# Optimization experiments

Hardware: AMD Instinct MI355X
Metric: run time of the kernel (lower is better)

## Reference

```python
import jax, jax.numpy as jnp
import numpy as np

ETA = 0.5  # from init_kwargs; eta >= 0 branch
N = 16777216

def setup_inputs() -> dict:
    key = jax.random.key(0)
    k1, k2 = jax.random.split(key)
    outputs = jax.random.normal(k1, (N,), dtype=jnp.float32)
    # PNU targets in {-1, 0, 1}
    targets = jax.random.randint(k2, (N,), 0, 3, dtype=jnp.int32) - 1
    p_ratio = jnp.array([0.4, 0.6], dtype=jnp.float32)
    return {"outputs": outputs, "targets": targets, "p_ratio": p_ratio}

def reference(outputs, targets, p_ratio):
    y = outputs.reshape(-1)
    t = targets.reshape(-1).astype(y.dtype)

    # masks (computed once, fused)
    idx_p = jnp.maximum(t, 0.0)          # positive examples
    idx_n = jnp.maximum(-t, 0.0)         # negative examples
    idx_u = 1.0 - jnp.abs(t)             # unlabeled examples

    sig_neg = jax.nn.sigmoid(-y)         # loss_func(-y)
    sig_pos = jax.nn.sigmoid(y)          # loss_func(-(-y))

    n_p = jnp.maximum(1.0, jnp.sum(idx_p))
    n_n = jnp.maximum(1.0, jnp.sum(idx_n))
    n_u = jnp.maximum(1.0, jnp.sum(idx_u))

    R_P_plus  = jnp.sum(idx_p * sig_neg) / n_p
    R_P_minus = jnp.sum(idx_p * sig_pos) / n_p
    R_N_minus = jnp.sum(idx_n * sig_pos) / n_n
    R_U_minus = jnp.sum(idx_u * sig_pos) / n_u

    R_PN = p_ratio[0] * R_P_plus + p_ratio[1] * R_N_minus
    R_PU = p_ratio[0] * (R_P_plus - R_P_minus) + R_U_minus

    # eta >= 0 branch
    return (1.0 - ETA) * R_PN + ETA * R_PU
```

## Files before the change

### kernel.cpp

```cpp
#include <hip/hip_runtime.h>

#define ETA 0.5f
#define NBLOCKS 2048
#define NTHREADS 256

__device__ __forceinline__ float wave_reduce_sum(float v) {
#pragma unroll
    for (int off = 32; off > 0; off >>= 1)
        v += __shfl_down(v, off, 64);
    return v;
}

__global__ __launch_bounds__(NTHREADS) void pnu_partial_kernel(
    const float* __restrict__ y, const int* __restrict__ t,
    float* __restrict__ partials, int n, int nblocks) {
    const int nvec = n >> 2;
    const float4* __restrict__ y4 = reinterpret_cast<const float4*>(y);
    const int4* __restrict__ t4 = reinterpret_cast<const int4*>(t);

    float sPp = 0.f, sPm = 0.f, sNm = 0.f, sUm = 0.f;
    float cP = 0.f, cN = 0.f, cU = 0.f;

    const int stride = gridDim.x * blockDim.x;
    for (int i = blockIdx.x * blockDim.x + threadIdx.x; i < nvec; i += stride) {
        float4 yv = y4[i];
        int4 tv = t4[i];
        float ys[4] = {yv.x, yv.y, yv.z, yv.w};
        int   ts[4] = {tv.x, tv.y, tv.z, tv.w};
#pragma unroll
        for (int j = 0; j < 4; ++j) {
            float s = __builtin_amdgcn_rcpf(1.0f + __expf(-ys[j]));
            int tt = ts[j];
            float isP = (tt == 1)  ? 1.0f : 0.0f;
            float isN = (tt == -1) ? 1.0f : 0.0f;
            float isU = (tt == 0)  ? 1.0f : 0.0f;
            sPp += isP * (1.0f - s);
            sPm += isP * s;
            sNm += isN * s;
            sUm += isU * s;
            cP += isP; cN += isN; cU += isU;
        }
    }

    if (blockIdx.x == 0 && threadIdx.x == 0) {
        for (int i = (nvec << 2); i < n; ++i) {
            float s = __builtin_amdgcn_rcpf(1.0f + __expf(-y[i]));
            int tt = t[i];
            float isP = (tt == 1)  ? 1.0f : 0.0f;
            float isN = (tt == -1) ? 1.0f : 0.0f;
            float isU = (tt == 0)  ? 1.0f : 0.0f;
            sPp += isP * (1.0f - s);
            sPm += isP * s;
            sNm += isN * s;
            sUm += isU * s;
            cP += isP; cN += isN; cU += isU;
        }
    }

    float vals[7] = {sPp, sPm, sNm, sUm, cP, cN, cU};
    __shared__ float red[NTHREADS / 64][7];
    const int lane = threadIdx.x & 63;
    const int wave = threadIdx.x >> 6;
#pragma unroll
    for (int k = 0; k < 7; ++k) {
        float r = wave_reduce_sum(vals[k]);
        if (lane == 0) red[wave][k] = r;
    }
    __syncthreads();
    if (threadIdx.x < 7) {
        float r = 0.f;
#pragma unroll
        for (int w = 0; w < NTHREADS / 64; ++w) r += red[w][threadIdx.x];
        partials[threadIdx.x * nblocks + blockIdx.x] = r;
    }
}

__global__ __launch_bounds__(NTHREADS) void pnu_final_kernel(
    const float* __restrict__ partials, const float* __restrict__ p_ratio,
    float* __restrict__ out, int nblocks) {
    float acc[7] = {0.f, 0.f, 0.f, 0.f, 0.f, 0.f, 0.f};
    for (int i = threadIdx.x; i < nblocks; i += blockDim.x) {
#pragma unroll
        for (int k = 0; k < 7; ++k) acc[k] += partials[k * nblocks + i];
    }
    __shared__ float red[NTHREADS / 64][7];
    const int lane = threadIdx.x & 63;
    const int wave = threadIdx.x >> 6;
#pragma unroll
    for (int k = 0; k < 7; ++k) {
        float r = wave_reduce_sum(acc[k]);
        if (lane == 0) red[wave][k] = r;
    }
    __syncthreads();
    if (threadIdx.x == 0) {
        float tot[7];
#pragma unroll
        for (int k = 0; k < 7; ++k) {
            float r = 0.f;
#pragma unroll
            for (int w = 0; w < NTHREADS / 64; ++w) r += red[w][k];
            tot[k] = r;
        }
        const float sPp = tot[0], sPm = tot[1], sNm = tot[2], sUm = tot[3];
        const float nP = fmaxf(1.0f, tot[4]);
        const float nN = fmaxf(1.0f, tot[5]);
        const float nU = fmaxf(1.0f, tot[6]);

        const float R_P_plus  = sPp / nP;
        const float R_P_minus = sPm / nP;
        const float R_N_minus = sNm / nN;
        const float R_U_minus = sUm / nU;

        const float pi0 = p_ratio[0], pi1 = p_ratio[1];
        const float R_PN = pi0 * R_P_plus + pi1 * R_N_minus;
        const float R_PU = pi0 * (R_P_plus - R_P_minus) + R_U_minus;

        out[0] = (1.0f - ETA) * R_PN + ETA * R_PU;
    }
}

extern "C" void kernel_launch(void* const* d_in, const int* in_sizes, int n_in,
                              void* d_out, int out_size, void* d_ws, size_t ws_size,
                              hipStream_t stream) {
    const float* y = (const float*)d_in[0];
    const int* t = (const int*)d_in[1];
    const float* p_ratio = (const float*)d_in[2];
    float* out = (float*)d_out;
    float* partials = (float*)d_ws;

    const int n = in_sizes[0];
    int nblocks = NBLOCKS;
    size_t need = (size_t)nblocks * 7 * sizeof(float);
    while (need > ws_size && nblocks > 64) { nblocks >>= 1; need = (size_t)nblocks * 7 * sizeof(float); }

    pnu_partial_kernel<<<nblocks, NTHREADS, 0, stream>>>(y, t, partials, n, nblocks);
    pnu_final_kernel<<<1, NTHREADS, 0, stream>>>(partials, p_ratio, out, nblocks);
}
```

Before: 34.02 us.

## Launch one block per chunk, unroll loads, reduce via algebraic accumulators

Replaces the seven per-class accumulators with five (sum of sigmoid, t*s, |t|*s, sum t, sum |t|) and recovers the per-class sums algebraically in the final kernel. The grid now has one block per 4096-element chunk (about 4096 blocks instead of 2048). Each thread issues four float4 and four int4 loads up front to raise memory-level parallelism. The final kernel uses 1024 threads to reduce the larger partials array. The algebraic recovery adds some float cancellation risk, and the single final block has more partials to read.

```diff
diff --git a/kernel.cpp b/kernel.cpp
--- a/kernel.cpp
+++ b/kernel.cpp
@@ -1,8 +1,10 @@
 #include <hip/hip_runtime.h>
 
 #define ETA 0.5f
-#define NBLOCKS 2048
 #define NTHREADS 256
+#define UNROLL 4
+#define CHUNK (NTHREADS * UNROLL)
+#define NACC 5
 
 __device__ __forceinline__ float wave_reduce_sum(float v) {
 #pragma unroll
@@ -11,63 +13,69 @@
     return v;
 }
 
+__device__ __forceinline__ void pnu_accum(float yy, int tt,
+                                          float& sAll, float& sT, float& sA,
+                                          float& cT, float& cA) {
+    float s = __builtin_amdgcn_rcpf(1.0f + __expf(-yy));
+    float tf = (float)tt;
+    float ta = fabsf(tf);
+    sAll += s;
+    sT = fmaf(tf, s, sT);
+    sA = fmaf(ta, s, sA);
+    cT += tf;
+    cA += ta;
+}
+
 __global__ __launch_bounds__(NTHREADS) void pnu_partial_kernel(
     const float* __restrict__ y, const int* __restrict__ t,
-    float* __restrict__ partials, int n, int nblocks) {
+    float* __restrict__ partials, int n, int nblocks, int nfull) {
     const int nvec = n >> 2;
     const float4* __restrict__ y4 = reinterpret_cast<const float4*>(y);
     const int4* __restrict__ t4 = reinterpret_cast<const int4*>(t);
 
-    float sPp = 0.f, sPm = 0.f, sNm = 0.f, sUm = 0.f;
-    float cP = 0.f, cN = 0.f, cU = 0.f;
+    float sAll = 0.f, sT = 0.f, sA = 0.f, cT = 0.f, cA = 0.f;
 
-    const int stride = gridDim.x * blockDim.x;
-    for (int i = blockIdx.x * blockDim.x + threadIdx.x; i < nvec; i += stride) {
-        float4 yv = y4[i];
-        int4 tv = t4[i];
-        float ys[4] = {yv.x, yv.y, yv.z, yv.w};
-        int   ts[4] = {tv.x, tv.y, tv.z, tv.w};
+    for (int c = blockIdx.x; c < nfull; c += gridDim.x) {
+        const int base = c * CHUNK + threadIdx.x;
+        float4 yv[UNROLL];
+        int4 tv[UNROLL];
 #pragma unroll
-        for (int j = 0; j < 4; ++j) {
-            float s = __builtin_amdgcn_rcpf(1.0f + __expf(-ys[j]));
-            int tt = ts[j];
-            float isP = (tt == 1)  ? 1.0f : 0.0f;
-            float isN = (tt == -1) ? 1.0f : 0.0f;
-            float isU = (tt == 0)  ? 1.0f : 0.0f;
-            sPp += isP * (1.0f - s);
-            sPm += isP * s;
-            sNm += isN * s;
-            sUm += isU * s;
-            cP += isP; cN += isN; cU += isU;
+        for (int u = 0; u < UNROLL; ++u) yv[u] = y4[base + u * NTHREADS];
+#pragma unroll
+        for (int u = 0; u < UNROLL; ++u) tv[u] = t4[base + u * NTHREADS];
+#pragma unroll
+        for (int u = 0; u < UNROLL; ++u) {
+            pnu_accum(yv[u].x, tv[u].x, sAll, sT, sA, cT, cA);
+            pnu_accum(yv[u].y, tv[u].y, sAll, sT, sA, cT, cA);
+            pnu_accum(yv[u].z, tv[u].z, sAll, sT, sA, cT, cA);
+            pnu_accum(yv[u].w, tv[u].w, sAll, sT, sA, cT, cA);
         }
     }
 
-    if (blockIdx.x == 0 && threadIdx.x == 0) {
-        for (int i = (nvec << 2); i < n; ++i) {
-            float s = __builtin_amdgcn_rcpf(1.0f + __expf(-y[i]));
-            int tt = t[i];
-            float isP = (tt == 1)  ? 1.0f : 0.0f;
-            float isN = (tt == -1) ? 1.0f : 0.0f;
-            float isU = (tt == 0)  ? 1.0f : 0.0f;
-            sPp += isP * (1.0f - s);
-            sPm += isP * s;
-            sNm += isN * s;
-            sUm += isU * s;
-            cP += isP; cN += isN; cU += isU;
+    if (blockIdx.x == gridDim.x - 1) {
+        for (int i = nfull * CHUNK + threadIdx.x; i < nvec; i += NTHREADS) {
+            float4 yv = y4[i];
+            int4 tv = t4[i];
+            pnu_accum(yv.x, tv.x, sAll, sT, sA, cT, cA);
+            pnu_accum(yv.y, tv.y, sAll, sT, sA, cT, cA);
+            pnu_accum(yv.z, tv.z, sAll, sT, sA, cT, cA);
+            pnu_accum(yv.w, tv.w, sAll, sT, sA, cT, cA);
         }
+        for (int i = (nvec << 2) + threadIdx.x; i < n; i += NTHREADS)
+            pnu_accum(y[i], t[i], sAll, sT, sA, cT, cA);
     }
 
-    float vals[7] = {sPp, sPm, sNm, sUm, cP, cN, cU};
-    __shared__ float red[NTHREADS / 64][7];
+    float vals[NACC] = {sAll, sT, sA, cT, cA};
+    __shared__ float red[NTHREADS / 64][NACC];
     const int lane = threadIdx.x & 63;
     const int wave = threadIdx.x >> 6;
 #pragma unroll
-    for (int k = 0; k < 7; ++k) {
+    for (int k = 0; k < NACC; ++k) {
         float r = wave_reduce_sum(vals[k]);
         if (lane == 0) red[wave][k] = r;
     }
     __syncthreads();
-    if (threadIdx.x < 7) {
+    if (threadIdx.x < NACC) {
         float r = 0.f;
 #pragma unroll
         for (int w = 0; w < NTHREADS / 64; ++w) r += red[w][threadIdx.x];
@@ -75,36 +83,48 @@
     }
 }
 
-__global__ __launch_bounds__(NTHREADS) void pnu_final_kernel(
+#define FTHREADS 1024
+
+__global__ __launch_bounds__(FTHREADS) void pnu_final_kernel(
     const float* __restrict__ partials, const float* __restrict__ p_ratio,
-    float* __restrict__ out, int nblocks) {
-    float acc[7] = {0.f, 0.f, 0.f, 0.f, 0.f, 0.f, 0.f};
-    for (int i = threadIdx.x; i < nblocks; i += blockDim.x) {
+    float* __restrict__ out, int nblocks, int n) {
+    float acc[NACC] = {0.f, 0.f, 0.f, 0.f, 0.f};
+    for (int i = threadIdx.x; i < nblocks; i += FTHREADS) {
 #pragma unroll
-        for (int k = 0; k < 7; ++k) acc[k] += partials[k * nblocks + i];
+        for (int k = 0; k < NACC; ++k) acc[k] += partials[k * nblocks + i];
     }
-    __shared__ float red[NTHREADS / 64][7];
+    __shared__ float red[FTHREADS / 64][NACC];
     const int lane = threadIdx.x & 63;
     const int wave = threadIdx.x >> 6;
 #pragma unroll
-    for (int k = 0; k < 7; ++k) {
+    for (int k = 0; k < NACC; ++k) {
         float r = wave_reduce_sum(acc[k]);
         if (lane == 0) red[wave][k] = r;
     }
     __syncthreads();
     if (threadIdx.x == 0) {
-        float tot[7];
+        float tot[NACC];
 #pragma unroll
-        for (int k = 0; k < 7; ++k) {
+        for (int k = 0; k < NACC; ++k) {
             float r = 0.f;
 #pragma unroll
-            for (int w = 0; w < NTHREADS / 64; ++w) r += red[w][k];
+            for (int w = 0; w < FTHREADS / 64; ++w) r += red[w][k];
             tot[k] = r;
         }
-        const float sPp = tot[0], sPm = tot[1], sNm = tot[2], sUm = tot[3];
-        const float nP = fmaxf(1.0f, tot[4]);
-        const float nN = fmaxf(1.0f, tot[5]);
-        const float nU = fmaxf(1.0f, tot[6]);
+        const float sAll = tot[0], sT = tot[1], sA = tot[2];
+        const float cT = tot[3], cA = tot[4];
+
+        const float cP = 0.5f * (cA + cT);
+        const float cN = 0.5f * (cA - cT);
+        const float cU = (float)n - cA;
+        const float sPm = 0.5f * (sA + sT);
+        const float sNm = 0.5f * (sA - sT);
+        const float sUm = sAll - sA;
+        const float sPp = cP - sPm;
+
+        const float nP = fmaxf(1.0f, cP);
+        const float nN = fmaxf(1.0f, cN);
+        const float nU = fmaxf(1.0f, cU);
 
         const float R_P_plus  = sPp / nP;
         const float R_P_minus = sPm / nP;
@@ -129,10 +149,16 @@
     float* partials = (float*)d_ws;
 
     const int n = in_sizes[0];
-    int nblocks = NBLOCKS;
-    size_t need = (size_t)nblocks * 7 * sizeof(float);
-    while (need > ws_size && nblocks > 64) { nblocks >>= 1; need = (size_t)nblocks * 7 * sizeof(float); }
+    const int nvec = n >> 2;
+    const int nfull = nvec / CHUNK;
+    const bool tail = (nfull * CHUNK * 4) < n;
+    int nblocks = nfull + (tail ? 1 : 0);
+    if (nblocks < 1) nblocks = 1;
 
-    pnu_partial_kernel<<<nblocks, NTHREADS, 0, stream>>>(y, t, partials, n, nblocks);
-    pnu_final_kernel<<<1, NTHREADS, 0, stream>>>(partials, p_ratio, out, nblocks);
+    int maxblocks = (int)(ws_size / (NACC * sizeof(float)));
+    if (maxblocks < 1) maxblocks = 1;
+    if (nblocks > maxblocks) nblocks = maxblocks;
+
+    pnu_partial_kernel<<<nblocks, NTHREADS, 0, stream>>>(y, t, partials, n, nblocks, nfull);
+    pnu_final_kernel<<<1, FTHREADS, 0, stream>>>(partials, p_ratio, out, nblocks, n);
 }
```

Result: faster. 30.43 us (-10.6%).
